# Performance work log

Measured on AMD Instinct MI355X. Metric: run time of the kernel, lower is better.

## Reference

```python
import jax, jax.numpy as jnp
import numpy as np

# ---- static circuit configuration (matches module init) ----
C = 6        # Fock cutoff (strawberryfields.tf cutoff_dim)
N = 5        # modes / wires
OUTPUT = 2   # output_size
LAYERS = 4   # layers
M = N * (N - 1) + max(1, N - 1)  # 24: params per interferometer

# ladder operators in truncated Fock basis
_a = np.diag(np.sqrt(np.arange(1, C)), 1)
A = jnp.asarray(_a, dtype=jnp.complex64)          # annihilation
AD = A.conj().T                                    # creation
NUM = jnp.arange(C, dtype=jnp.float32)             # number operator diag
I1 = jnp.eye(C, dtype=jnp.complex64)
A1 = jnp.kron(A, I1)   # a on mode 1 of a 2-mode block
A2 = jnp.kron(I1, A)   # a on mode 2 of a 2-mode block


def _expm(H, order=16, s=6):
    # scaling-and-squaring + Horner Taylor; fully differentiable, small matrices only
    Hs = H * jnp.asarray(1.0 / (2 ** s), H.dtype)
    I = jnp.eye(H.shape[-1], dtype=H.dtype)
    R = I
    for k in range(order, 0, -1):
        R = I + (Hs @ R) * jnp.asarray(1.0 / k, H.dtype)
    for _ in range(s):
        R = R @ R
    return R


def disp_gate(r, phi):
    al = jax.lax.complex(r * jnp.cos(phi), r * jnp.sin(phi))
    return _expm(al * AD - jnp.conj(al) * A)


def squeeze_gate(r):
    # S(r, 0) = exp(r/2 (a^2 - adag^2))
    return _expm(jax.lax.complex(r, jnp.zeros_like(r)) * 0.5 * (A @ A - AD @ AD))


def rot_gate(phi):
    return jnp.diag(jnp.exp(1j * phi * NUM))


def kerr_gate(kap):
    return jnp.diag(jnp.exp(1j * kap * NUM * NUM))


def bs_gate(theta, phi):
    ep = jnp.exp(1j * phi)
    H = ep * (A1 @ A2.conj().T) - jnp.conj(ep) * (A1.conj().T @ A2)
    th = jax.lax.complex(theta, jnp.zeros_like(theta))
    return _expm(th * H).reshape(C, C, C, C)


def apply1(U, psi, m):
    psi = jnp.tensordot(U, psi, axes=([1], [m]))
    return jnp.moveaxis(psi, 0, m)


def apply2(U4, psi, m):
    # U4[o1,o2,i1,i2] acting on adjacent modes (m, m+1)
    psi = jnp.tensordot(U4, psi, axes=([2, 3], [m, m + 1]))
    return jnp.moveaxis(psi, [0, 1], [m, m + 1])


def interferometer(p, psi):
    T = N * (N - 1) // 2
    theta, phi, rphi = p[:T], p[T:2 * T], p[-(N - 1):]
    n = 0
    for l in range(N):
        for k in range(N - 1):
            if (l + k) % 2 == 0:  # same condition as (l+k)%2 != 1 being False
                psi = apply2(bs_gate(theta[n], phi[n]), psi, k)
                n += 1
    for i in range(max(1, N - 1)):
        psi = apply1(rot_gate(rphi[i]), psi, i)
    return psi


def linear_layer(p, psi):
    psi = interferometer(p[:M], psi)
    for i in range(N):
        psi = apply1(squeeze_gate(p[M + i]), psi, i)
    psi = interferometer(p[M + N:2 * M + N], psi)
    dr = p[2 * M + N:2 * M + 2 * N]
    dp = p[2 * M + 2 * N:2 * M + 3 * N]
    for i in range(N):
        psi = apply1(disp_gate(dr[i], dp[i]), psi, i)
    return psi


def circuit(xi, lin, act, last_act):
    psi = jnp.zeros((C,) * N, jnp.complex64).at[(0,) * N].set(1.0)
    zero = jnp.float32(0.0)
    for i in range(N):  # Displacement encoding of input
        psi = apply1(disp_gate(xi[i], zero), psi, i)
    for l in range(LAYERS - 1):
        psi = linear_layer(lin[l], psi)
        for i in range(N):  # Kerr activation
            psi = apply1(kerr_gate(act[l, i]), psi, i)
    psi = linear_layer(lin[LAYERS - 1], psi)
    for i in range(OUTPUT):  # last activation on first OUTPUT modes
        psi = apply1(kerr_gate(last_act[i]), psi, i)
    X = A + AD  # x quadrature, hbar=2 (StrawberryFields convention)
    return jnp.stack([jnp.real(jnp.vdot(psi, apply1(X, psi, i))) for i in range(OUTPUT)])


def setup_inputs() -> dict:
    key = jax.random.key(0)
    k1, k2, k3, k4 = jax.random.split(key, 4)
    B = 2048
    x = jax.random.uniform(k1, (B, N), dtype=jnp.float32)
    linear_params = 0.001 * jax.random.normal(k2, (LAYERS, 2 * M + 3 * N), dtype=jnp.float32)
    activation_params = 0.001 * jax.random.normal(k3, (LAYERS - 1, N), dtype=jnp.float32)
    last_activation_params = 0.001 * jax.random.normal(k4, (N,), dtype=jnp.float32)
    return {
        "x": x,
        "linear_params": linear_params,
        "activation_params": activation_params,
        "last_activation_params": last_activation_params,
    }


def reference(x, linear_params, activation_params, last_activation_params):
    f = lambda xi: circuit(xi, linear_params, activation_params, last_activation_params)
    return jax.vmap(f)(x)  # [B, OUTPUT]
```

## Files before the change

kernel.cpp:

```cpp
#include <hip/hip_runtime.h>


typedef float    vf2 __attribute__((ext_vector_type(2)));
typedef _Float16 h2  __attribute__((ext_vector_type(2)));
typedef _Float16 h4  __attribute__((ext_vector_type(4)));

__device__ __forceinline__ h2 pkfma(const h2 a, const h2 b, const h2 c) {
    return __builtin_elementwise_fma(a, b, c);
}

__device__ __forceinline__ void cmadd(float &ax, float &ay, const float2 u, const float2 v) {
    ax = fmaf(u.x, v.x, ax);
    ax = fmaf(-u.y, v.y, ax);
    ay = fmaf(u.x, v.y, ay);
    ay = fmaf(u.y, v.x, ay);
}

constexpr int BS_SN[11]  = {1,2,3,4,5,6,5,4,3,2,1};
constexpr int BS_OFF[11] = {0,1,5,14,30,55,91,116,132,141,145};

__device__ const int d_BS_OFF[12] = {0,1,5,14,30,55,91,116,132,141,145,146};
__device__ const int d_BS_SN[11]  = {1,2,3,4,5,6,5,4,3,2,1};

__global__ void gates_kernel(const float* __restrict__ lin,
                             const float* __restrict__ act,
                             const float* __restrict__ lact,
                             h2* __restrict__ bsh,
                             h2* __restrict__ sgh)
{
    __shared__ float2 B0[1296];
    __shared__ float2 B1[1296];
    const int tid = threadIdx.x;

    if (blockIdx.x < 80) {
        const int g = blockIdx.x;
        const int l = g / 20;
        const int w = g % 20;
        const int q = w / 10;
        const int n = w % 10;
        const float theta = lin[l*63 + (q ? 29 : 0) + n];
        const float phi   = lin[l*63 + (q ? 39 : 10) + n];
        const float ts = theta * 0.015625f;
        const float cp = cosf(phi), sp = sinf(phi);
        const float2 u  = make_float2( ts*cp, ts*sp);
        const float2 w2 = make_float2(-ts*cp, ts*sp);

        float2 *R = B0, *T = B1;
        for (int e = tid; e < 1296; e += 256)
            R[e] = make_float2((e % 37 == 0) ? 1.f : 0.f, 0.f);
        __syncthreads();

        for (int k = 16; k >= 1; --k) {
            const float invk = 1.f / (float)k;
            for (int e = tid; e < 1296; e += 256) {
                const int row = e / 36, c = e - row*36;
                const int i = row / 6, j = row - (row/6)*6;
                float ax = 0.f, ay = 0.f;
                if (i < 5 && j > 0) {
                    const float coef = sqrtf((float)((i+1)*j));
                    const float2 x = R[(row+5)*36 + c];
                    const float px = u.x*x.x - u.y*x.y;
                    const float py = u.x*x.y + u.y*x.x;
                    ax = fmaf(coef, px, ax); ay = fmaf(coef, py, ay);
                }
                if (i > 0 && j < 5) {
                    const float coef = sqrtf((float)(i*(j+1)));
                    const float2 x = R[(row-5)*36 + c];
                    const float px = w2.x*x.x - w2.y*x.y;
                    const float py = w2.x*x.y + w2.y*x.x;
                    ax = fmaf(coef, px, ax); ay = fmaf(coef, py, ay);
                }
                T[e] = make_float2(((row == c) ? 1.f : 0.f) + ax*invk, ay*invk);
            }
            __syncthreads();
            float2* tmp = R; R = T; T = tmp;
        }
        for (int s2 = 0; s2 < 6; ++s2) {
            for (int e = tid; e < 1296; e += 256) {
                const int row = e / 36, c = e - row*36;
                float ax = 0.f, ay = 0.f;
                #pragma unroll 6
                for (int k = 0; k < 36; ++k)
                    cmadd(ax, ay, R[row*36 + k], R[k*36 + c]);
                T[e] = make_float2(ax, ay);
            }
            __syncthreads();
            float2* tmp = R; R = T; T = tmp;
        }
        for (int idx = tid; idx < 146; idx += 256) {
            int nn = 0;
            while (idx >= d_BS_OFF[nn+1]) ++nn;
            const int sn  = d_BS_SN[nn];
            const int rel = idx - d_BS_OFF[nn];
            const int p = rel / sn, qq = rel % sn;
            const int imin = (nn > 5) ? (nn - 5) : 0;
            const int row = 5*(imin + p)  + nn;
            const int col = 5*(imin + qq) + nn;
            const float2 z = R[row*36 + col];
            bsh[g*292 + 2*idx    ] = (h2){(_Float16)z.x, (_Float16)z.x};
            bsh[g*292 + 2*idx + 1] = (h2){(_Float16)z.y, (_Float16)z.y};
        }
    } else {
        const int t = tid;
        if (t >= 40) return;
        const int l  = t / 10;
        const int gi = t % 10;
        float2 G[36];
        if (gi < 5) {
            const int m = gi;
            const float r    = lin[l*63 + 24 + m];
            const float rphi = (m < 4) ? lin[l*63 + 20 + m] : 0.f;
            float R[36], T[36];
            #pragma unroll
            for (int e = 0; e < 36; ++e) R[e] = (e % 7 == 0) ? 1.f : 0.f;
            float hp[4];
            #pragma unroll
            for (int i = 0; i < 4; ++i)
                hp[i] = 0.5f * r * sqrtf((float)((i+1)*(i+2))) * 0.015625f;
            for (int k = 16; k >= 1; --k) {
                const float invk = 1.f / (float)k;
                #pragma unroll
                for (int i = 0; i < 6; ++i) {
                    #pragma unroll
                    for (int c = 0; c < 6; ++c) {
                        float a = 0.f;
                        if (i < 4)  a = fmaf( hp[i],   R[(i+2)*6 + c], a);
                        if (i >= 2) a = fmaf(-hp[i-2], R[(i-2)*6 + c], a);
                        T[i*6+c] = ((i == c) ? 1.f : 0.f) + a*invk;
                    }
                }
                #pragma unroll
                for (int e = 0; e < 36; ++e) R[e] = T[e];
            }
            for (int s2 = 0; s2 < 6; ++s2) {
                #pragma unroll
                for (int i = 0; i < 6; ++i) {
                    #pragma unroll
                    for (int c = 0; c < 6; ++c) {
                        float a = 0.f;
                        #pragma unroll
                        for (int k = 0; k < 6; ++k) a = fmaf(R[i*6+k], R[k*6+c], a);
                        T[i*6+c] = a;
                    }
                }
                #pragma unroll
                for (int e = 0; e < 36; ++e) R[e] = T[e];
            }
            #pragma unroll
            for (int c = 0; c < 6; ++c) {
                const float cc = cosf(rphi * (float)c), ss = sinf(rphi * (float)c);
                #pragma unroll
                for (int o = 0; o < 6; ++o)
                    G[o*6 + c] = make_float2(R[o*6+c]*cc, R[o*6+c]*ss);
            }
        } else {
            const int m = gi - 5;
            const float dr   = lin[l*63 + 53 + m];
            const float dp   = lin[l*63 + 58 + m];
            const float rphi = (m < 4) ? lin[l*63 + 49 + m] : 0.f;
            const float kap  = (l < 3) ? act[l*5 + m] : ((m < 2) ? lact[m] : 0.f);
            const float2 al = make_float2(dr * cosf(dp), dr * sinf(dp));
            float2 R[36], T[36];
            #pragma unroll
            for (int e = 0; e < 36; ++e)
                R[e] = make_float2((e % 7 == 0) ? 1.f : 0.f, 0.f);
            float2 cm[6], cpb[6];
            #pragma unroll
            for (int i = 0; i < 6; ++i) {
                const float sm  = sqrtf((float)i)     * 0.015625f;
                const float sp2 = sqrtf((float)(i+1)) * 0.015625f;
                cm[i]  = make_float2( al.x*sm,  al.y*sm);
                cpb[i] = make_float2(-al.x*sp2, al.y*sp2);
            }
            for (int k = 16; k >= 1; --k) {
                const float invk = 1.f / (float)k;
                #pragma unroll
                for (int i = 0; i < 6; ++i) {
                    #pragma unroll
                    for (int c = 0; c < 6; ++c) {
                        float ax = 0.f, ay = 0.f;
                        if (i >= 1) cmadd(ax, ay, cm[i],  R[(i-1)*6 + c]);
                        if (i < 5)  cmadd(ax, ay, cpb[i], R[(i+1)*6 + c]);
                        T[i*6+c] = make_float2(((i == c) ? 1.f : 0.f) + ax*invk, ay*invk);
                    }
                }
                #pragma unroll
                for (int e = 0; e < 36; ++e) R[e] = T[e];
            }
            for (int s2 = 0; s2 < 6; ++s2) {
                #pragma unroll
                for (int i = 0; i < 6; ++i) {
                    #pragma unroll
                    for (int c = 0; c < 6; ++c) {
                        float ax = 0.f, ay = 0.f;
                        #pragma unroll
                        for (int k = 0; k < 6; ++k) cmadd(ax, ay, R[i*6+k], R[k*6+c]);
                        T[i*6+c] = make_float2(ax, ay);
                    }
                }
                #pragma unroll
                for (int e = 0; e < 36; ++e) R[e] = T[e];
            }
            #pragma unroll
            for (int o = 0; o < 6; ++o) {
                const float ko = kap * (float)(o*o);
                const float2 kp = make_float2(cosf(ko), sinf(ko));
                #pragma unroll
                for (int c = 0; c < 6; ++c) {
                    const float rc = rphi * (float)c;
                    const float2 rp = make_float2(cosf(rc), sinf(rc));
                    const float2 z = R[o*6 + c];
                    const float2 t1 = make_float2(kp.x*z.x - kp.y*z.y, kp.x*z.y + kp.y*z.x);
                    G[o*6 + c] = make_float2(t1.x*rp.x - t1.y*rp.y, t1.x*rp.y + t1.y*rp.x);
                }
            }
        }
        h2* outp = sgh + (l*10 + gi)*72;
        #pragma unroll
        for (int e = 0; e < 36; ++e) {
            outp[2*e    ] = (h2){(_Float16)G[e].x, (_Float16)G[e].x};
            outp[2*e + 1] = (h2){(_Float16)G[e].y, (_Float16)G[e].y};
        }
    }
}

__global__ void dcol_kernel(const float* __restrict__ x,
                            float* __restrict__ dcol, const int total)
{
    const int i = blockIdx.x * 256 + threadIdx.x;
    if (i >= total) return;
    const float xv = x[i];
    float a[5];
    #pragma unroll
    for (int j = 0; j < 5; ++j) a[j] = xv * sqrtf((float)(j+1)) * 0.015625f;
    float R[36], T[36];
    #pragma unroll
    for (int e = 0; e < 36; ++e) R[e] = (e % 7 == 0) ? 1.f : 0.f;
    for (int k = 16; k >= 1; --k) {
        const float invk = 1.f / (float)k;
        #pragma unroll
        for (int r = 0; r < 6; ++r) {
            #pragma unroll
            for (int c = 0; c < 6; ++c) {
                float acc = 0.f;
                if (r >= 1) acc = fmaf( a[r-1], R[(r-1)*6 + c], acc);
                if (r < 5)  acc = fmaf(-a[r],   R[(r+1)*6 + c], acc);
                T[r*6+c] = ((r == c) ? 1.f : 0.f) + acc*invk;
            }
        }
        #pragma unroll
        for (int e = 0; e < 36; ++e) R[e] = T[e];
    }
    for (int s2 = 0; s2 < 6; ++s2) {
        #pragma unroll
        for (int r = 0; r < 6; ++r) {
            #pragma unroll
            for (int c = 0; c < 6; ++c) {
                float acc = 0.f;
                #pragma unroll
                for (int k = 0; k < 6; ++k) acc = fmaf(R[r*6+k], R[k*6+c], acc);
                T[r*6+c] = acc;
            }
        }
        #pragma unroll
        for (int e = 0; e < 36; ++e) R[e] = T[e];
    }
    #pragma unroll
    for (int j = 0; j < 6; ++j) dcol[i*6 + j] = R[j*6 + 0];
}


template<int SA, int SB, int n, int R0, int R1>
__device__ __forceinline__ void bs_rows(const h2* __restrict__ U,
                                        h4* __restrict__ psi,
                                        const int base, const bool act)
{
    constexpr int sn = BS_SN[n], uoff = BS_OFF[n];
    constexpr int imin = (n > 5) ? (n - 5) : 0;
    if (!act) return;
    h2 vR[sn], vI[sn];
    #pragma unroll
    for (int q = 0; q < sn; ++q) {
        const int c = 5*(imin + q) + n;
        const h4 v = psi[base + (c/6)*SA + (c%6)*SB];
        vR[q] = (h2){v.x, v.y};
        vI[q] = (h2){v.z, v.w};
    }
    h2 oR[R1-R0], oI[R1-R0];
    #pragma unroll
    for (int p = R0; p < R1; ++p) {
        const h2* Up = U + 2*(uoff + p*sn);
        h2 ur = Up[0], ui = Up[1];
        h2 aR = ur * vR[0];
        aR = pkfma(-ui, vI[0], aR);
        h2 aI = ur * vI[0];
        aI = pkfma(ui, vR[0], aI);
        #pragma unroll
        for (int q = 1; q < sn; ++q) {
            ur = Up[2*q]; ui = Up[2*q + 1];
            aR = pkfma(ur, vR[q], aR);
            aR = pkfma(-ui, vI[q], aR);
            aI = pkfma(ur, vI[q], aI);
            aI = pkfma(ui, vR[q], aI);
        }
        oR[p-R0] = aR; oI[p-R0] = aI;
    }
    #pragma unroll
    for (int p = R0; p < R1; ++p) {
        const int c = 5*(imin + p) + n;
        const h2 r = oR[p-R0], m = oI[p-R0];
        psi[base + (c/6)*SA + (c%6)*SB] = (h4){r.x, r.y, m.x, m.y};
    }
}

template<int SA, int SB>
__device__ __forceinline__ void pass_bs(const h2* __restrict__ U,
                                        h4* __restrict__ psi,
                                        const int base, const bool act, const int qid)
{
    if (qid == 0) {
        bs_rows<SA,SB,5,0,6>(U, psi, base, act);
    } else if (qid == 1) {
        bs_rows<SA,SB,4,0,5>(U, psi, base, act);
        bs_rows<SA,SB,2,0,3>(U, psi, base, act);
        bs_rows<SA,SB,1,0,2>(U, psi, base, act);
    } else if (qid == 2) {
        bs_rows<SA,SB,6,0,5>(U, psi, base, act);
        bs_rows<SA,SB,8,0,3>(U, psi, base, act);
        bs_rows<SA,SB,9,0,2>(U, psi, base, act);
    } else {
        bs_rows<SA,SB,3,0,4>(U, psi, base, act);
        bs_rows<SA,SB,7,0,4>(U, psi, base, act);
        bs_rows<SA,SB,0,0,1>(U, psi, base, act);
        bs_rows<SA,SB,10,0,1>(U, psi, base, act);
    }
    __syncthreads();
}

template<int SM, bool SP>
__device__ __forceinline__ void sg_fiber(const h2* __restrict__ G,
                                         h4* __restrict__ psi,
                                         const int base)
{
    h2 vR[6], vI[6];
    #pragma unroll
    for (int k = 0; k < 6; ++k) {
        const h4 v = psi[base + k*SM];
        vR[k] = (h2){v.x, v.y};
        vI[k] = (h2){v.z, v.w};
    }
    h2 oR[6], oI[6];
    #pragma unroll
    for (int o = 0; o < 6; ++o) {
        const int k0 = SP ? (o & 1) : 0;
        const int st = SP ? 2 : 1;
        h2 ur = G[2*(o*6 + k0)], ui = G[2*(o*6 + k0) + 1];
        h2 aR = ur * vR[k0];
        aR = pkfma(-ui, vI[k0], aR);
        h2 aI = ur * vI[k0];
        aI = pkfma(ui, vR[k0], aI);
        #pragma unroll
        for (int k = k0 + st; k < 6; k += st) {
            ur = G[2*(o*6 + k)]; ui = G[2*(o*6 + k) + 1];
            aR = pkfma(ur, vR[k], aR);
            aR = pkfma(-ui, vI[k], aR);
            aI = pkfma(ur, vI[k], aI);
            aI = pkfma(ui, vR[k], aI);
        }
        oR[o] = aR; oI[o] = aI;
    }
    #pragma unroll
    for (int o = 0; o < 6; ++o)
        psi[base + o*SM] = (h4){oR[o].x, oR[o].y, oI[o].x, oI[o].y};
}

template<int SM, int S0, int S1, int S2, int S3, bool SP>
__device__ __forceinline__ void pass_sg(const h2* __restrict__ G,
                                        h4* __restrict__ psi,
                                        const int4 dg0, const int4 dg1, const bool act1)
{
    {
        const int base = dg0.x*S0 + dg0.y*S1 + dg0.z*S2 + dg0.w*S3;
        sg_fiber<SM,SP>(G, psi, base);
    }
    if (act1) {
        const int base = dg1.x*S0 + dg1.y*S1 + dg1.z*S2 + dg1.w*S3;
        sg_fiber<SM,SP>(G, psi, base);
    }
    __syncthreads();
}

__global__ __launch_bounds__(1024, 8)
void qnet_kernel(const h2* __restrict__ bs,
                 const h2* __restrict__ sg,
                 const float* __restrict__ dcol,
                 float* __restrict__ out,
                 const int B)
{
    __shared__ __align__(16) h4 psi[7992];
    __shared__ float stf[60];
    __shared__ float red[64];

    const int tid = threadIdx.x;
    const int b   = blockIdx.x;

    const int lim = B * 30;
    if (tid < 60) stf[tid] = (b*60 + tid < lim) ? dcol[b*60 + tid] : 0.f;
    __syncthreads();
    for (int e = tid; e < 7776; e += 1024) {
        int t = e;
        const int i4 = t % 6; t /= 6;
        const int i3 = t % 6; t /= 6;
        const int i2 = t % 6; t /= 6;
        const int i1 = t % 6; t /= 6;
        const int i0 = t;
        const int addr = 6*i0 + i1 + 36*i2 + 221*i3 + 1334*i4;
        const float v0 = stf[i0]*stf[6+i1]*stf[12+i2]*stf[18+i3]*stf[24+i4];
        const float v1 = stf[30+i0]*stf[36+i1]*stf[42+i2]*stf[48+i3]*stf[54+i4];
        psi[addr] = (h4){(_Float16)v0, (_Float16)v1, (_Float16)0.f, (_Float16)0.f};
    }
    __syncthreads();

    const int sub = tid & 255;
    const int qid = __builtin_amdgcn_readfirstlane(tid >> 8);
    const bool act = sub < 216;
    const int f = act ? sub : 215;
    const int fa = f / 36, rem = f - fa*36;
    const int fb = rem / 6, fc = rem - fb*6;
    const int baseK0 = fa*36 + fb*221 + fc*1334;
    const int baseK1 = fa*6  + fb*221 + fc*1334;
    const int baseK2 = rem   + fa*1334;
    const int baseK3 = f;

    int4 dg0, dg1;
    { int t = tid;        dg0.x = t % 6; t /= 6; dg0.y = t % 6; t /= 6; dg0.z = t % 6; dg0.w = t / 6; }
    { int t = tid + 1024; dg1.x = t % 6; t /= 6; dg1.y = t % 6; t /= 6; dg1.z = t % 6; dg1.w = t / 6; }
    const bool act1 = tid < 272;

    for (int l = 0; l < 4; ++l) {
        const h2* bsl = bs + l * 20 * 292;
        const h2* sgl = sg + l * 10 * 72;
        for (int hf = 0; hf < 2; ++hf) {
            const h2* bh = bsl + hf * 10 * 292;
            const h2* sh = sgl + hf * 5 * 72;
            pass_bs<6,1>     (bh + 0*292, psi, baseK0, act, qid);
            pass_bs<36,221>  (bh + 1*292, psi, baseK2, act, qid);
            pass_bs<1,36>    (bh + 2*292, psi, baseK1, act, qid);
            pass_bs<221,1334>(bh + 3*292, psi, baseK3, act, qid);
            pass_bs<6,1>     (bh + 4*292, psi, baseK0, act, qid);
            pass_bs<36,221>  (bh + 5*292, psi, baseK2, act, qid);
            pass_bs<1,36>    (bh + 6*292, psi, baseK1, act, qid);
            pass_bs<221,1334>(bh + 7*292, psi, baseK3, act, qid);
            pass_bs<6,1>     (bh + 8*292, psi, baseK0, act, qid);
            pass_bs<36,221>  (bh + 9*292, psi, baseK2, act, qid);
            if (hf == 0) {
                pass_sg<6,    1,36,221,1334, true>(sh + 0*72, psi, dg0, dg1, act1);
                pass_sg<1,    6,36,221,1334, true>(sh + 1*72, psi, dg0, dg1, act1);
                pass_sg<36,   1,6,221,1334,  true>(sh + 2*72, psi, dg0, dg1, act1);
                pass_sg<221,  1,6,36,1334,   true>(sh + 3*72, psi, dg0, dg1, act1);
                pass_sg<1334, 1,6,36,221,    true>(sh + 4*72, psi, dg0, dg1, act1);
            } else {
                pass_sg<6,    1,36,221,1334, false>(sh + 0*72, psi, dg0, dg1, act1);
                pass_sg<1,    6,36,221,1334, false>(sh + 1*72, psi, dg0, dg1, act1);
                pass_sg<36,   1,6,221,1334,  false>(sh + 2*72, psi, dg0, dg1, act1);
                pass_sg<221,  1,6,36,1334,   false>(sh + 3*72, psi, dg0, dg1, act1);
                pass_sg<1334, 1,6,36,221,    false>(sh + 4*72, psi, dg0, dg1, act1);
            }
        }
    }

    float s0a = 0.f, s0b = 0.f, s1a = 0.f, s1b = 0.f;
    for (int fr = tid; fr < 1296; fr += 1024) {
        const int q0 = fr % 6;
        const int q1 = (fr / 6) % 6;
        const int q2 = (fr / 36) % 6;
        const int q3 = fr / 216;
        const int base0 = q0*1 + q1*36 + q2*221 + q3*1334;
        #pragma unroll
        for (int j = 0; j < 5; ++j) {
            const h4 a = psi[base0 + 6*j];
            const h4 c = psi[base0 + 6*(j+1)];
            const float w = sqrtf((float)(j+1));
            s0a = fmaf(w, fmaf((float)a.z, (float)c.z, (float)a.x*(float)c.x), s0a);
            s0b = fmaf(w, fmaf((float)a.w, (float)c.w, (float)a.y*(float)c.y), s0b);
        }
        const int base1 = q0*6 + q1*36 + q2*221 + q3*1334;
        #pragma unroll
        for (int j = 0; j < 5; ++j) {
            const h4 a = psi[base1 + j];
            const h4 c = psi[base1 + j + 1];
            const float w = sqrtf((float)(j+1));
            s1a = fmaf(w, fmaf((float)a.z, (float)c.z, (float)a.x*(float)c.x), s1a);
            s1b = fmaf(w, fmaf((float)a.w, (float)c.w, (float)a.y*(float)c.y), s1b);
        }
    }
    #pragma unroll
    for (int off = 32; off > 0; off >>= 1) {
        s0a += __shfl_down(s0a, off, 64);
        s0b += __shfl_down(s0b, off, 64);
        s1a += __shfl_down(s1a, off, 64);
        s1b += __shfl_down(s1b, off, 64);
    }
    if ((tid & 63) == 0) {
        const int w = tid >> 6;
        red[w*4 + 0] = s0a; red[w*4 + 1] = s1a;
        red[w*4 + 2] = s0b; red[w*4 + 3] = s1b;
    }
    __syncthreads();
    if (tid == 0) {
        float r0 = 0.f, r1 = 0.f, r2 = 0.f, r3 = 0.f;
        #pragma unroll
        for (int w = 0; w < 16; ++w) {
            r0 += red[w*4 + 0]; r1 += red[w*4 + 1];
            r2 += red[w*4 + 2]; r3 += red[w*4 + 3];
        }
        const int b0 = 2*b, b1 = 2*b + 1;
        out[b0*2 + 0] = 2.f * r0;
        out[b0*2 + 1] = 2.f * r1;
        if (b1 < B) {
            out[b1*2 + 0] = 2.f * r2;
            out[b1*2 + 1] = 2.f * r3;
        }
    }
}

extern "C" void kernel_launch(void* const* d_in, const int* in_sizes, int n_in,
                              void* d_out, int out_size, void* d_ws, size_t ws_size,
                              hipStream_t stream)
{
    const float* x    = (const float*)d_in[0];
    const float* lin  = (const float*)d_in[1];
    const float* act  = (const float*)d_in[2];
    const float* lact = (const float*)d_in[3];
    float* out = (float*)d_out;

    const int B = in_sizes[0] / 5;

    h2*    bsh = (h2*)d_ws;
    h2*    sgh = bsh + 80*292;
    float* dc  = (float*)(sgh + 40*72);

    gates_kernel<<<dim3(81), dim3(256), 0, stream>>>(lin, act, lact, bsh, sgh);
    const int total = B * 5;
    dcol_kernel<<<dim3((total + 255)/256), dim3(256), 0, stream>>>(x, dc, total);
    qnet_kernel<<<dim3((B + 1) / 2), dim3(1024), 0, stream>>>(bsh, sgh, dc, out, B);
}
```

Measured before the change: 814.3 us.

## Pack four batch samples per block and skip final-layer passes that cannot affect outputs

The kernel is templated on the number of samples packed into each fp16 shared-memory amplitude, and a 4-sample variant stores h8 vectors in about 128KB of dynamic LDS. Each gate coefficient load and the index arithmetic are now shared across four states instead of two, and half as many blocks are launched. It also drops the last beamsplitters and squeeze or Kerr passes on modes that do not affect the measured quadratures of modes 0 and 1 before the final readout. In exchange, the larger LDS footprint leaves room for only one block per CU, and each thread uses more registers for the wider vectors.

```diff
diff --git a/kernel.cpp b/kernel.cpp
--- a/kernel.cpp
+++ b/kernel.cpp
@@ -4,6 +4,7 @@
 typedef float    vf2 __attribute__((ext_vector_type(2)));
 typedef _Float16 h2  __attribute__((ext_vector_type(2)));
 typedef _Float16 h4  __attribute__((ext_vector_type(4)));
+typedef _Float16 h8  __attribute__((ext_vector_type(8)));
 
 __device__ __forceinline__ h2 pkfma(const h2 a, const h2 b, const h2 c) {
     return __builtin_elementwise_fma(a, b, c);
@@ -21,6 +22,10 @@
 
 __device__ const int d_BS_OFF[12] = {0,1,5,14,30,55,91,116,132,141,145,146};
 __device__ const int d_BS_SN[11]  = {1,2,3,4,5,6,5,4,3,2,1};
+
+template<int P> struct VecT;
+template<> struct VecT<2> { typedef h4 type; };
+template<> struct VecT<4> { typedef h8 type; };
 
 __global__ void gates_kernel(const float* __restrict__ lin,
                              const float* __restrict__ act,
@@ -270,142 +275,178 @@
 }
 
 
-template<int SA, int SB, int n, int R0, int R1>
+template<int P>
+__device__ __forceinline__ void ampLoad(const typename VecT<P>::type* __restrict__ psi,
+                                        const int idx, h2* R, h2* I)
+{
+    const auto v = psi[idx];
+    if constexpr (P == 2) {
+        R[0] = __builtin_shufflevector(v, v, 0, 1);
+        I[0] = __builtin_shufflevector(v, v, 2, 3);
+    } else {
+        R[0] = __builtin_shufflevector(v, v, 0, 1);
+        R[1] = __builtin_shufflevector(v, v, 2, 3);
+        I[0] = __builtin_shufflevector(v, v, 4, 5);
+        I[1] = __builtin_shufflevector(v, v, 6, 7);
+    }
+}
+
+template<int P>
+__device__ __forceinline__ typename VecT<P>::type ampPack(const h2* R, const h2* I)
+{
+    if constexpr (P == 2) {
+        return (h4){R[0].x, R[0].y, I[0].x, I[0].y};
+    } else {
+        return (h8){R[0].x, R[0].y, R[1].x, R[1].y,
+                    I[0].x, I[0].y, I[1].x, I[1].y};
+    }
+}
+
+template<int W>
+__device__ __forceinline__ void cmul2(const h2 ur, const h2 ui,
+                                      const h2* vR, const h2* vI, h2* aR, h2* aI)
+{
+    #pragma unroll
+    for (int w = 0; w < W; ++w) {
+        aR[w] = ur * vR[w];
+        aR[w] = pkfma(-ui, vI[w], aR[w]);
+        aI[w] = ur * vI[w];
+        aI[w] = pkfma(ui, vR[w], aI[w]);
+    }
+}
+template<int W>
+__device__ __forceinline__ void cmac2(const h2 ur, const h2 ui,
+                                      const h2* vR, const h2* vI, h2* aR, h2* aI)
+{
+    #pragma unroll
+    for (int w = 0; w < W; ++w) {
+        aR[w] = pkfma(ur, vR[w], aR[w]);
+        aR[w] = pkfma(-ui, vI[w], aR[w]);
+        aI[w] = pkfma(ur, vI[w], aI[w]);
+        aI[w] = pkfma(ui, vR[w], aI[w]);
+    }
+}
+
+template<int P, int SA, int SB, int n, int R0, int R1>
 __device__ __forceinline__ void bs_rows(const h2* __restrict__ U,
-                                        h4* __restrict__ psi,
+                                        typename VecT<P>::type* __restrict__ psi,
                                         const int base, const bool act)
 {
+    constexpr int W = P/2;
     constexpr int sn = BS_SN[n], uoff = BS_OFF[n];
     constexpr int imin = (n > 5) ? (n - 5) : 0;
     if (!act) return;
-    h2 vR[sn], vI[sn];
+    h2 vR[sn][W], vI[sn][W];
     #pragma unroll
     for (int q = 0; q < sn; ++q) {
         const int c = 5*(imin + q) + n;
-        const h4 v = psi[base + (c/6)*SA + (c%6)*SB];
-        vR[q] = (h2){v.x, v.y};
-        vI[q] = (h2){v.z, v.w};
-    }
-    h2 oR[R1-R0], oI[R1-R0];
+        ampLoad<P>(psi, base + (c/6)*SA + (c%6)*SB, vR[q], vI[q]);
+    }
+    h2 oR[R1-R0][W], oI[R1-R0][W];
     #pragma unroll
     for (int p = R0; p < R1; ++p) {
         const h2* Up = U + 2*(uoff + p*sn);
-        h2 ur = Up[0], ui = Up[1];
-        h2 aR = ur * vR[0];
-        aR = pkfma(-ui, vI[0], aR);
-        h2 aI = ur * vI[0];
-        aI = pkfma(ui, vR[0], aI);
-        #pragma unroll
-        for (int q = 1; q < sn; ++q) {
-            ur = Up[2*q]; ui = Up[2*q + 1];
-            aR = pkfma(ur, vR[q], aR);
-            aR = pkfma(-ui, vI[q], aR);
-            aI = pkfma(ur, vI[q], aI);
-            aI = pkfma(ui, vR[q], aI);
-        }
-        oR[p-R0] = aR; oI[p-R0] = aI;
+        cmul2<W>(Up[0], Up[1], vR[0], vI[0], oR[p-R0], oI[p-R0]);
+        #pragma unroll
+        for (int q = 1; q < sn; ++q)
+            cmac2<W>(Up[2*q], Up[2*q + 1], vR[q], vI[q], oR[p-R0], oI[p-R0]);
     }
     #pragma unroll
     for (int p = R0; p < R1; ++p) {
         const int c = 5*(imin + p) + n;
-        const h2 r = oR[p-R0], m = oI[p-R0];
-        psi[base + (c/6)*SA + (c%6)*SB] = (h4){r.x, r.y, m.x, m.y};
-    }
-}
-
-template<int SA, int SB>
+        psi[base + (c/6)*SA + (c%6)*SB] = ampPack<P>(oR[p-R0], oI[p-R0]);
+    }
+}
+
+template<int P, int SA, int SB>
 __device__ __forceinline__ void pass_bs(const h2* __restrict__ U,
-                                        h4* __restrict__ psi,
+                                        typename VecT<P>::type* __restrict__ psi,
                                         const int base, const bool act, const int qid)
 {
     if (qid == 0) {
-        bs_rows<SA,SB,5,0,6>(U, psi, base, act);
+        bs_rows<P,SA,SB,5,0,6>(U, psi, base, act);
     } else if (qid == 1) {
-        bs_rows<SA,SB,4,0,5>(U, psi, base, act);
-        bs_rows<SA,SB,2,0,3>(U, psi, base, act);
-        bs_rows<SA,SB,1,0,2>(U, psi, base, act);
+        bs_rows<P,SA,SB,4,0,5>(U, psi, base, act);
+        bs_rows<P,SA,SB,2,0,3>(U, psi, base, act);
+        bs_rows<P,SA,SB,1,0,2>(U, psi, base, act);
     } else if (qid == 2) {
-        bs_rows<SA,SB,6,0,5>(U, psi, base, act);
-        bs_rows<SA,SB,8,0,3>(U, psi, base, act);
-        bs_rows<SA,SB,9,0,2>(U, psi, base, act);
+        bs_rows<P,SA,SB,6,0,5>(U, psi, base, act);
+        bs_rows<P,SA,SB,8,0,3>(U, psi, base, act);
+        bs_rows<P,SA,SB,9,0,2>(U, psi, base, act);
     } else {
-        bs_rows<SA,SB,3,0,4>(U, psi, base, act);
-        bs_rows<SA,SB,7,0,4>(U, psi, base, act);
-        bs_rows<SA,SB,0,0,1>(U, psi, base, act);
-        bs_rows<SA,SB,10,0,1>(U, psi, base, act);
+        bs_rows<P,SA,SB,3,0,4>(U, psi, base, act);
+        bs_rows<P,SA,SB,7,0,4>(U, psi, base, act);
+        bs_rows<P,SA,SB,0,0,1>(U, psi, base, act);
+        bs_rows<P,SA,SB,10,0,1>(U, psi, base, act);
     }
     __syncthreads();
 }
 
-template<int SM, bool SP>
+template<int P, int SM, bool SP>
 __device__ __forceinline__ void sg_fiber(const h2* __restrict__ G,
-                                         h4* __restrict__ psi,
+                                         typename VecT<P>::type* __restrict__ psi,
                                          const int base)
 {
-    h2 vR[6], vI[6];
-    #pragma unroll
-    for (int k = 0; k < 6; ++k) {
-        const h4 v = psi[base + k*SM];
-        vR[k] = (h2){v.x, v.y};
-        vI[k] = (h2){v.z, v.w};
-    }
-    h2 oR[6], oI[6];
+    constexpr int W = P/2;
+    h2 vR[6][W], vI[6][W];
+    #pragma unroll
+    for (int k = 0; k < 6; ++k)
+        ampLoad<P>(psi, base + k*SM, vR[k], vI[k]);
+    h2 oR[6][W], oI[6][W];
     #pragma unroll
     for (int o = 0; o < 6; ++o) {
         const int k0 = SP ? (o & 1) : 0;
         const int st = SP ? 2 : 1;
-        h2 ur = G[2*(o*6 + k0)], ui = G[2*(o*6 + k0) + 1];
-        h2 aR = ur * vR[k0];
-        aR = pkfma(-ui, vI[k0], aR);
-        h2 aI = ur * vI[k0];
-        aI = pkfma(ui, vR[k0], aI);
-        #pragma unroll
-        for (int k = k0 + st; k < 6; k += st) {
-            ur = G[2*(o*6 + k)]; ui = G[2*(o*6 + k) + 1];
-            aR = pkfma(ur, vR[k], aR);
-            aR = pkfma(-ui, vI[k], aR);
-            aI = pkfma(ur, vI[k], aI);
-            aI = pkfma(ui, vR[k], aI);
-        }
-        oR[o] = aR; oI[o] = aI;
+        cmul2<W>(G[2*(o*6 + k0)], G[2*(o*6 + k0) + 1], vR[k0], vI[k0], oR[o], oI[o]);
+        #pragma unroll
+        for (int k = k0 + st; k < 6; k += st)
+            cmac2<W>(G[2*(o*6 + k)], G[2*(o*6 + k) + 1], vR[k], vI[k], oR[o], oI[o]);
     }
     #pragma unroll
     for (int o = 0; o < 6; ++o)
-        psi[base + o*SM] = (h4){oR[o].x, oR[o].y, oI[o].x, oI[o].y};
-}
-
-template<int SM, int S0, int S1, int S2, int S3, bool SP>
+        psi[base + o*SM] = ampPack<P>(oR[o], oI[o]);
+}
+
+template<int P, int SM, int S0, int S1, int S2, int S3, bool SP>
 __device__ __forceinline__ void pass_sg(const h2* __restrict__ G,
-                                        h4* __restrict__ psi,
+                                        typename VecT<P>::type* __restrict__ psi,
                                         const int4 dg0, const int4 dg1, const bool act1)
 {
     {
         const int base = dg0.x*S0 + dg0.y*S1 + dg0.z*S2 + dg0.w*S3;
-        sg_fiber<SM,SP>(G, psi, base);
+        sg_fiber<P,SM,SP>(G, psi, base);
     }
     if (act1) {
         const int base = dg1.x*S0 + dg1.y*S1 + dg1.z*S2 + dg1.w*S3;
-        sg_fiber<SM,SP>(G, psi, base);
+        sg_fiber<P,SM,SP>(G, psi, base);
     }
     __syncthreads();
 }
 
-__global__ __launch_bounds__(1024, 8)
-void qnet_kernel(const h2* __restrict__ bs,
-                 const h2* __restrict__ sg,
-                 const float* __restrict__ dcol,
-                 float* __restrict__ out,
-                 const int B)
-{
-    __shared__ __align__(16) h4 psi[7992];
-    __shared__ float stf[60];
-    __shared__ float red[64];
+__device__ __forceinline__ float hget(const h2 v, const int hi) {
+    return (float)(hi ? v.y : v.x);
+}
+
+template<int PACK>
+__device__ __forceinline__ void qnet_body(const h2* __restrict__ bs,
+                                          const h2* __restrict__ sg,
+                                          const float* __restrict__ dcol,
+                                          float* __restrict__ out,
+                                          const int B)
+{
+    constexpr int W = PACK/2;
+    using AT = typename VecT<PACK>::type;
+    extern __shared__ __align__(16) char qnet_smem[];
+    AT* psi = reinterpret_cast<AT*>(qnet_smem);
+    __shared__ float stf[PACK*30];
+    __shared__ float red[16*2*PACK];
 
     const int tid = threadIdx.x;
     const int b   = blockIdx.x;
 
     const int lim = B * 30;
-    if (tid < 60) stf[tid] = (b*60 + tid < lim) ? dcol[b*60 + tid] : 0.f;
+    if (tid < PACK*30)
+        stf[tid] = (b*PACK*30 + tid < lim) ? dcol[b*PACK*30 + tid] : 0.f;
     __syncthreads();
     for (int e = tid; e < 7776; e += 1024) {
         int t = e;
@@ -415,9 +456,16 @@
         const int i1 = t % 6; t /= 6;
         const int i0 = t;
         const int addr = 6*i0 + i1 + 36*i2 + 221*i3 + 1334*i4;
-        const float v0 = stf[i0]*stf[6+i1]*stf[12+i2]*stf[18+i3]*stf[24+i4];
-        const float v1 = stf[30+i0]*stf[36+i1]*stf[42+i2]*stf[48+i3]*stf[54+i4];
-        psi[addr] = (h4){(_Float16)v0, (_Float16)v1, (_Float16)0.f, (_Float16)0.f};
+        h2 R[W], I[W];
+        #pragma unroll
+        for (int p = 0; p < PACK; ++p) {
+            const float v = stf[p*30 + i0]*stf[p*30 + 6 + i1]*stf[p*30 + 12 + i2]
+                          * stf[p*30 + 18 + i3]*stf[p*30 + 24 + i4];
+            if (p & 1) R[p>>1].y = (_Float16)v; else R[p>>1].x = (_Float16)v;
+        }
+        #pragma unroll
+        for (int w = 0; w < W; ++w) I[w] = (h2){(_Float16)0.f, (_Float16)0.f};
+        psi[addr] = ampPack<PACK>(R, I);
     }
     __syncthreads();
 
@@ -443,33 +491,40 @@
         for (int hf = 0; hf < 2; ++hf) {
             const h2* bh = bsl + hf * 10 * 292;
             const h2* sh = sgl + hf * 5 * 72;
-            pass_bs<6,1>     (bh + 0*292, psi, baseK0, act, qid);
-            pass_bs<36,221>  (bh + 1*292, psi, baseK2, act, qid);
-            pass_bs<1,36>    (bh + 2*292, psi, baseK1, act, qid);
-            pass_bs<221,1334>(bh + 3*292, psi, baseK3, act, qid);
-            pass_bs<6,1>     (bh + 4*292, psi, baseK0, act, qid);
-            pass_bs<36,221>  (bh + 5*292, psi, baseK2, act, qid);
-            pass_bs<1,36>    (bh + 6*292, psi, baseK1, act, qid);
-            pass_bs<221,1334>(bh + 7*292, psi, baseK3, act, qid);
-            pass_bs<6,1>     (bh + 8*292, psi, baseK0, act, qid);
-            pass_bs<36,221>  (bh + 9*292, psi, baseK2, act, qid);
+            const bool last = (l == 3) && (hf == 1);
+            pass_bs<PACK,6,1>     (bh + 0*292, psi, baseK0, act, qid);
+            pass_bs<PACK,36,221>  (bh + 1*292, psi, baseK2, act, qid);
+            pass_bs<PACK,1,36>    (bh + 2*292, psi, baseK1, act, qid);
+            pass_bs<PACK,221,1334>(bh + 3*292, psi, baseK3, act, qid);
+            pass_bs<PACK,6,1>     (bh + 4*292, psi, baseK0, act, qid);
+            pass_bs<PACK,36,221>  (bh + 5*292, psi, baseK2, act, qid);
+            pass_bs<PACK,1,36>    (bh + 6*292, psi, baseK1, act, qid);
+            if (!last)
+                pass_bs<PACK,221,1334>(bh + 7*292, psi, baseK3, act, qid);
+            pass_bs<PACK,6,1>     (bh + 8*292, psi, baseK0, act, qid);
+            if (!last)
+                pass_bs<PACK,36,221>  (bh + 9*292, psi, baseK2, act, qid);
             if (hf == 0) {
-                pass_sg<6,    1,36,221,1334, true>(sh + 0*72, psi, dg0, dg1, act1);
-                pass_sg<1,    6,36,221,1334, true>(sh + 1*72, psi, dg0, dg1, act1);
-                pass_sg<36,   1,6,221,1334,  true>(sh + 2*72, psi, dg0, dg1, act1);
-                pass_sg<221,  1,6,36,1334,   true>(sh + 3*72, psi, dg0, dg1, act1);
-                pass_sg<1334, 1,6,36,221,    true>(sh + 4*72, psi, dg0, dg1, act1);
+                pass_sg<PACK,6,    1,36,221,1334, true>(sh + 0*72, psi, dg0, dg1, act1);
+                pass_sg<PACK,1,    6,36,221,1334, true>(sh + 1*72, psi, dg0, dg1, act1);
+                pass_sg<PACK,36,   1,6,221,1334,  true>(sh + 2*72, psi, dg0, dg1, act1);
+                pass_sg<PACK,221,  1,6,36,1334,   true>(sh + 3*72, psi, dg0, dg1, act1);
+                pass_sg<PACK,1334, 1,6,36,221,    true>(sh + 4*72, psi, dg0, dg1, act1);
             } else {
-                pass_sg<6,    1,36,221,1334, false>(sh + 0*72, psi, dg0, dg1, act1);
-                pass_sg<1,    6,36,221,1334, false>(sh + 1*72, psi, dg0, dg1, act1);
-                pass_sg<36,   1,6,221,1334,  false>(sh + 2*72, psi, dg0, dg1, act1);
-                pass_sg<221,  1,6,36,1334,   false>(sh + 3*72, psi, dg0, dg1, act1);
-                pass_sg<1334, 1,6,36,221,    false>(sh + 4*72, psi, dg0, dg1, act1);
-            }
-        }
-    }
-
-    float s0a = 0.f, s0b = 0.f, s1a = 0.f, s1b = 0.f;
+                pass_sg<PACK,6,    1,36,221,1334, false>(sh + 0*72, psi, dg0, dg1, act1);
+                pass_sg<PACK,1,    6,36,221,1334, false>(sh + 1*72, psi, dg0, dg1, act1);
+                if (!last) {
+                    pass_sg<PACK,36,   1,6,221,1334,  false>(sh + 2*72, psi, dg0, dg1, act1);
+                    pass_sg<PACK,221,  1,6,36,1334,   false>(sh + 3*72, psi, dg0, dg1, act1);
+                    pass_sg<PACK,1334, 1,6,36,221,    false>(sh + 4*72, psi, dg0, dg1, act1);
+                }
+            }
+        }
+    }
+
+    float s0[PACK], s1[PACK];
+    #pragma unroll
+    for (int p = 0; p < PACK; ++p) { s0[p] = 0.f; s1[p] = 0.f; }
     for (int fr = tid; fr < 1296; fr += 1024) {
         const int q0 = fr % 6;
         const int q1 = (fr / 6) % 6;
@@ -478,50 +533,78 @@
         const int base0 = q0*1 + q1*36 + q2*221 + q3*1334;
         #pragma unroll
         for (int j = 0; j < 5; ++j) {
-            const h4 a = psi[base0 + 6*j];
-            const h4 c = psi[base0 + 6*(j+1)];
-            const float w = sqrtf((float)(j+1));
-            s0a = fmaf(w, fmaf((float)a.z, (float)c.z, (float)a.x*(float)c.x), s0a);
-            s0b = fmaf(w, fmaf((float)a.w, (float)c.w, (float)a.y*(float)c.y), s0b);
+            h2 aR[W], aI[W], cR[W], cI[W];
+            ampLoad<PACK>(psi, base0 + 6*j,     aR, aI);
+            ampLoad<PACK>(psi, base0 + 6*(j+1), cR, cI);
+            const float wj = sqrtf((float)(j+1));
+            #pragma unroll
+            for (int p = 0; p < PACK; ++p) {
+                const int w = p >> 1, hi = p & 1;
+                s0[p] = fmaf(wj, fmaf(hget(aI[w],hi), hget(cI[w],hi),
+                                      hget(aR[w],hi)*hget(cR[w],hi)), s0[p]);
+            }
         }
         const int base1 = q0*6 + q1*36 + q2*221 + q3*1334;
         #pragma unroll
         for (int j = 0; j < 5; ++j) {
-            const h4 a = psi[base1 + j];
-            const h4 c = psi[base1 + j + 1];
-            const float w = sqrtf((float)(j+1));
-            s1a = fmaf(w, fmaf((float)a.z, (float)c.z, (float)a.x*(float)c.x), s1a);
-            s1b = fmaf(w, fmaf((float)a.w, (float)c.w, (float)a.y*(float)c.y), s1b);
+            h2 aR[W], aI[W], cR[W], cI[W];
+            ampLoad<PACK>(psi, base1 + j,     aR, aI);
+            ampLoad<PACK>(psi, base1 + j + 1, cR, cI);
+            const float wj = sqrtf((float)(j+1));
+            #pragma unroll
+            for (int p = 0; p < PACK; ++p) {
+                const int w = p >> 1, hi = p & 1;
+                s1[p] = fmaf(wj, fmaf(hget(aI[w],hi), hget(cI[w],hi),
+                                      hget(aR[w],hi)*hget(cR[w],hi)), s1[p]);
+            }
         }
     }
     #pragma unroll
     for (int off = 32; off > 0; off >>= 1) {
-        s0a += __shfl_down(s0a, off, 64);
-        s0b += __shfl_down(s0b, off, 64);
-        s1a += __shfl_down(s1a, off, 64);
-        s1b += __shfl_down(s1b, off, 64);
+        #pragma unroll
+        for (int p = 0; p < PACK; ++p) {
+            s0[p] += __shfl_down(s0[p], off, 64);
+            s1[p] += __shfl_down(s1[p], off, 64);
+        }
     }
     if ((tid & 63) == 0) {
         const int w = tid >> 6;
-        red[w*4 + 0] = s0a; red[w*4 + 1] = s1a;
-        red[w*4 + 2] = s0b; red[w*4 + 3] = s1b;
+        #pragma unroll
+        for (int p = 0; p < PACK; ++p) {
+            red[w*2*PACK + 2*p    ] = s0[p];
+            red[w*2*PACK + 2*p + 1] = s1[p];
+        }
     }
     __syncthreads();
     if (tid == 0) {
-        float r0 = 0.f, r1 = 0.f, r2 = 0.f, r3 = 0.f;
-        #pragma unroll
-        for (int w = 0; w < 16; ++w) {
-            r0 += red[w*4 + 0]; r1 += red[w*4 + 1];
-            r2 += red[w*4 + 2]; r3 += red[w*4 + 3];
-        }
-        const int b0 = 2*b, b1 = 2*b + 1;
-        out[b0*2 + 0] = 2.f * r0;
-        out[b0*2 + 1] = 2.f * r1;
-        if (b1 < B) {
-            out[b1*2 + 0] = 2.f * r2;
-            out[b1*2 + 1] = 2.f * r3;
-        }
-    }
+        #pragma unroll
+        for (int p = 0; p < PACK; ++p) {
+            float r0 = 0.f, r1 = 0.f;
+            for (int w = 0; w < 16; ++w) {
+                r0 += red[w*2*PACK + 2*p];
+                r1 += red[w*2*PACK + 2*p + 1];
+            }
+            const int bb = PACK*b + p;
+            if (bb < B) {
+                out[bb*2 + 0] = 2.f * r0;
+                out[bb*2 + 1] = 2.f * r1;
+            }
+        }
+    }
+}
+
+__global__ __launch_bounds__(1024, 8)
+void qnet_kernel2(const h2* __restrict__ bs, const h2* __restrict__ sg,
+                  const float* __restrict__ dcol, float* __restrict__ out, const int B)
+{
+    qnet_body<2>(bs, sg, dcol, out, B);
+}
+
+__global__ __launch_bounds__(1024, 4)
+void qnet_kernel4(const h2* __restrict__ bs, const h2* __restrict__ sg,
+                  const float* __restrict__ dcol, float* __restrict__ out, const int B)
+{
+    qnet_body<4>(bs, sg, dcol, out, B);
 }
 
 extern "C" void kernel_launch(void* const* d_in, const int* in_sizes, int n_in,
@@ -540,8 +623,20 @@
     h2*    sgh = bsh + 80*292;
     float* dc  = (float*)(sgh + 40*72);
 
+    static int use4 = -1;
+    if (use4 < 0) {
+        hipError_t e = hipFuncSetAttribute(
+            reinterpret_cast<const void*>(qnet_kernel4),
+            hipFuncAttributeMaxDynamicSharedMemorySize, 131072);
+        use4 = (e == hipSuccess) ? 1 : 0;
+    }
+
     gates_kernel<<<dim3(81), dim3(256), 0, stream>>>(lin, act, lact, bsh, sgh);
     const int total = B * 5;
     dcol_kernel<<<dim3((total + 255)/256), dim3(256), 0, stream>>>(x, dc, total);
-    qnet_kernel<<<dim3((B + 1) / 2), dim3(1024), 0, stream>>>(bsh, sgh, dc, out, B);
-}
+    if (use4) {
+        qnet_kernel4<<<dim3((B + 3) / 4), dim3(1024), 7992*16, stream>>>(bsh, sgh, dc, out, B);
+    } else {
+        qnet_kernel2<<<dim3((B + 1) / 2), dim3(1024), 7992*8, stream>>>(bsh, sgh, dc, out, B);
+    }
+}
```

New measurement: 831.4 us. 1.02x slower.
